# Kernel optimization log

Measured on AMD Instinct MI355X. Metric: run time of the kernel, lower is better.

Reference implementation:

```python
import jax, jax.numpy as jnp
import numpy as np

BANDWIDTH = 8.0

def setup_inputs() -> dict:
    key = jax.random.key(0)
    k1, k2 = jax.random.split(key)
    points = jax.random.normal(k1, (1, 8192, 32), dtype=jnp.float32)
    reference = jax.random.normal(k2, (1, 8192, 32), dtype=jnp.float32)
    return {"points": points, "reference": reference}

def reference(points, reference):
    # points: [B, N, D], reference: [B, M, D]
    # squared Euclidean distances via the expanded form to avoid the
    # O(B*N*M*D) difference tensor the original broadcasting would build
    x2 = jnp.sum(points * points, axis=-1)      # [B, N]
    y2 = jnp.sum(reference * reference, axis=-1)  # [B, M]
    xy = jnp.einsum('bnd,bmd->bnm', points, reference)  # [B, N, M]
    s_ij = x2[:, :, None] + y2[:, None, :] - 2.0 * xy   # [B, N, M]
    factor = jnp.float32(-1.0 / (2.0 * BANDWIDTH ** 2))
    k_ij = jnp.exp(s_ij * factor)               # [B, N, M] gaussian kernel
    nominator = jnp.einsum('bnm,bmd->bnd', k_ij, reference)
    denominator = jnp.sum(k_ij, axis=2, keepdims=True)  # [B, N, 1]
    return nominator / denominator
```

## Files before the change

kernel.cpp:

```cpp
#include <hip/hip_runtime.h>
#include <hip/hip_bf16.h>

#define D 32
#define FACTOR (-1.0f / 128.0f)
#define LOG2E  1.44269504088896340736f

typedef __attribute__((ext_vector_type(8)))  short bf16x8;
typedef __attribute__((ext_vector_type(16))) float f32x16;
typedef __attribute__((ext_vector_type(4)))  float f32x4;

#if __has_builtin(__builtin_amdgcn_exp2f)
#define EXP2(x) __builtin_amdgcn_exp2f(x)
#else
#define EXP2(x) exp2f(x)
#endif

__device__ __forceinline__ ushort bfr(float x) {
    __hip_bfloat16 h = __float2bfloat16(x);
    return *reinterpret_cast<ushort*>(&h);
}
__device__ __forceinline__ float bf2f(ushort u) {
    uint w = ((uint)u) << 16;
    return *reinterpret_cast<float*>(&w);
}
__device__ __forceinline__ uint pk2(float a, float b) {
    return (uint)bfr(a) | ((uint)bfr(b) << 16);
}

__global__ __launch_bounds__(256) void msk_prep(const float* __restrict__ X,
                                                const float* __restrict__ Y,
                                                ushort* __restrict__ Xb,
                                                ushort* __restrict__ Yb,
                                                ushort* __restrict__ yT,
                                                float* __restrict__ x2,
                                                float* __restrict__ y2,
                                                int N, int M) {
    const int t = blockIdx.x * 256 + threadIdx.x;
    const int i = t >> 2;
    const int c = t & 3;
    if (i >= N + M) return;
    const bool isX = (i < N);
    const int r = isX ? i : i - N;
    const float* src = (isX ? X : Y) + (size_t)r * D + c * 8;

    float4 va = *reinterpret_cast<const float4*>(src);
    float4 vb = *reinterpret_cast<const float4*>(src + 4);
    float f[8] = {va.x, va.y, va.z, va.w, vb.x, vb.y, vb.z, vb.w};

    ushort u[8];
    float s = 0.f;
#pragma unroll
    for (int k = 0; k < 8; ++k) {
        u[k] = bfr(f[k]);
        float g = bf2f(u[k]);
        s = fmaf(g, g, s);
    }
    s += __shfl_xor(s, 1);
    s += __shfl_xor(s, 2);

    uint w[4];
#pragma unroll
    for (int q = 0; q < 4; ++q) w[q] = (uint)u[2 * q] | ((uint)u[2 * q + 1] << 16);

    ushort* dstrow = (isX ? Xb : Yb) + (size_t)r * D + c * 8;
    *reinterpret_cast<uint4*>(dstrow) = *reinterpret_cast<const uint4*>(w);

    if (c == 0) (isX ? x2 : y2)[r] = s;

    if (!isX) {
#pragma unroll
        for (int k = 0; k < 8; ++k)
            yT[(size_t)(c * 8 + k) * M + r] = u[k];
    }
}

__global__ __launch_bounds__(256) void msk_main(const ushort* __restrict__ Xb,
                                                const ushort* __restrict__ Yb,
                                                const ushort* __restrict__ yT,
                                                const float* __restrict__ x2,
                                                const float* __restrict__ y2,
                                                float* __restrict__ pnom,
                                                float* __restrict__ pden,
                                                int N, int M, int chunk) {
    __shared__ uint4 lYb[2][64][4];
    __shared__ uint4 lYT[2][32][8];

    const int tid  = threadIdx.x;
    const int lane = tid & 63;
    const int wid  = tid >> 6;
    const int h    = lane >> 5;
    const int ln   = lane & 31;
    const int n0   = blockIdx.x * 128 + wid * 32;
    const int m0b  = blockIdx.y * chunk;
    const int ns   = chunk >> 6;

    const int rY = tid >> 2, cY = tid & 3;
    const int dT = tid >> 3, sT = tid & 7;

    const ushort* xrow = Xb + (size_t)(n0 + ln) * D + h * 8;
    const bf16x8 xf0 = *reinterpret_cast<const bf16x8*>(xrow);
    const bf16x8 xf1 = *reinterpret_cast<const bf16x8*>(xrow + 16);

    const float F2  = FACTOR * LOG2E;
    const float C2  = -2.0f * F2;
    const float xb2 = x2[n0 + ln] * F2;

    f32x16 nom = {};
    float den = 0.f;

    union Fu { uint u[4]; bf16x8 v; };

    uint4 ldYb, ldYT;
    auto issue_loads = [&](int step) {
        const int m = m0b + step * 64;
        ldYb = *(reinterpret_cast<const uint4*>(Yb + (size_t)(m + rY) * D) + cY);
        ldYT = *(reinterpret_cast<const uint4*>(yT + (size_t)dT * M + m) + sT);
    };
    auto stage = [&](int b) {
        lYb[b][rY][cY ^ (rY & 3)] = ldYb;
        lYT[b][dT][sT ^ (dT & 7)] = ldYT;
    };

    issue_loads(0);
    stage(0);
    if (ns > 1) issue_loads(1);

    for (int t = 0; t < ns; ++t) {
        __syncthreads();
        const int b  = t & 1;
        const int m0 = m0b + t * 64;

#pragma unroll
        for (int tA = 0; tA < 2; ++tA) {
            const int lr = tA * 32 + ln;
            const bf16x8 af0 = *reinterpret_cast<const bf16x8*>(
                &lYb[b][lr][(0 + h) ^ (ln & 3)]);
            const bf16x8 af1 = *reinterpret_cast<const bf16x8*>(
                &lYb[b][lr][(2 + h) ^ (ln & 3)]);

            f32x16 s = {};
            s = __builtin_amdgcn_mfma_f32_32x32x16_bf16(af0, xf0, s, 0, 0, 0);
            s = __builtin_amdgcn_mfma_f32_32x32x16_bf16(af1, xf1, s, 0, 0, 0);

            const int mt = m0 + tA * 32;
            uint pw[8];
#pragma unroll
            for (int r4 = 0; r4 < 4; ++r4) {
                f32x4 yv = *reinterpret_cast<const f32x4*>(y2 + mt + r4 * 8 + h * 4);
                float kq[4];
#pragma unroll
                for (int q = 0; q < 4; ++q)
                    kq[q] = EXP2(fmaf(s[r4 * 4 + q], C2, fmaf(yv[q], F2, xb2)));
                den += (kq[0] + kq[1]) + (kq[2] + kq[3]);
                pw[r4 * 2 + 0] = pk2(kq[0], kq[1]);
                pw[r4 * 2 + 1] = pk2(kq[2], kq[3]);
            }
            Fu pa0, pa1;
#pragma unroll
            for (int q = 0; q < 4; ++q) { pa0.u[q] = pw[q]; pa1.u[q] = pw[q + 4]; }

            const uint2* yr = reinterpret_cast<const uint2*>(&lYT[b][ln][0]);
            const int sw = ln & 7;
            Fu b0, b1;
            *reinterpret_cast<uint2*>(&b0.u[0]) = yr[((tA * 4 + 0) ^ sw) * 2 + h];
            *reinterpret_cast<uint2*>(&b0.u[2]) = yr[((tA * 4 + 1) ^ sw) * 2 + h];
            *reinterpret_cast<uint2*>(&b1.u[0]) = yr[((tA * 4 + 2) ^ sw) * 2 + h];
            *reinterpret_cast<uint2*>(&b1.u[2]) = yr[((tA * 4 + 3) ^ sw) * 2 + h];

            nom = __builtin_amdgcn_mfma_f32_32x32x16_bf16(pa0.v, b0.v, nom, 0, 0, 0);
            nom = __builtin_amdgcn_mfma_f32_32x32x16_bf16(pa1.v, b1.v, nom, 0, 0, 0);
        }

        if (t + 1 < ns) {
            stage((t + 1) & 1);
            if (t + 2 < ns) issue_loads(t + 2);
        }
    }

    den += __shfl_xor(den, 32);

    const size_t base = (size_t)blockIdx.y * N;
#pragma unroll
    for (int r = 0; r < 16; ++r) {
        const int row = (r & 3) + 8 * (r >> 2) + 4 * h;
        pnom[(base + n0 + row) * 32 + ln] = nom[r];
    }
    if (h == 0) pden[base + n0 + ln] = den;
}

__global__ __launch_bounds__(256) void msk_reduce(const float* __restrict__ pnom,
                                                  const float* __restrict__ pden,
                                                  float* __restrict__ out,
                                                  int N, int S) {
    const int t = blockIdx.x * blockDim.x + threadIdx.x;
    if (t >= N * 32) return;
    const int n = t >> 5;
    float nom = 0.f, den = 0.f;
    for (int s = 0; s < S; ++s) {
        nom += pnom[(size_t)s * N * 32 + t];
        den += pden[(size_t)s * N + n];
    }
    out[t] = nom / den;
}

extern "C" void kernel_launch(void* const* d_in, const int* in_sizes, int n_in,
                              void* d_out, int out_size, void* d_ws, size_t ws_size,
                              hipStream_t stream) {
    const float* X = (const float*)d_in[0];
    const float* Y = (const float*)d_in[1];
    float* out     = (float*)d_out;

    const int N = in_sizes[0] / D;
    const int M = in_sizes[1] / D;

    char* p = (char*)d_ws;
    ushort* Xb = (ushort*)p; p += (size_t)N * D * sizeof(ushort);
    ushort* Yb = (ushort*)p; p += (size_t)M * D * sizeof(ushort);
    ushort* yT = (ushort*)p; p += (size_t)M * D * sizeof(ushort);
    float*  x2 = (float*)p;  p += (size_t)N * sizeof(float);
    float*  y2 = (float*)p;  p += (size_t)M * sizeof(float);
    size_t used = (size_t)(p - (char*)d_ws);
    used = (used + 255) & ~(size_t)255;

    const size_t per_s = (size_t)N * 33 * sizeof(float);
    int S = 16;
    while (S > 1 && used + (size_t)S * per_s > ws_size) S >>= 1;
    const int chunk = M / S;

    float* pnom = (float*)((char*)d_ws + used);
    float* pden = pnom + (size_t)S * N * 32;

    msk_prep<<<dim3(((N + M) * 4 + 255) / 256), dim3(256), 0, stream>>>(
        X, Y, Xb, Yb, yT, x2, y2, N, M);

    msk_main<<<dim3(N / 128, S), dim3(256), 0, stream>>>(
        Xb, Yb, yT, x2, y2, pnom, pden, N, M, chunk);

    msk_reduce<<<dim3((N * 32 + 255) / 256), dim3(256), 0, stream>>>(
        pnom, pden, out, N, S);
}
```

Measured before the change: 91.41 us.

## Software-pipeline QK MFMA one tile ahead of exp and PV MFMA with setprio

Restructures the main loop so the distance GEMM for the next 64-row Y tile is issued right after the barrier, while the exp/pack and the numerator GEMM for the current tile run in between. Both 32-row subtiles are computed together, so their MFMAs are independent and interleaved. s_setprio raises wave priority around the MFMA bursts. The aim is to overlap matrix-core latency with the VALU exp work. The cost is higher register pressure from holding two extra accumulators (sA0/sA1).

```diff
diff --git a/kernel.cpp b/kernel.cpp
--- a/kernel.cpp
+++ b/kernel.cpp
@@ -107,7 +107,6 @@
 
     f32x16 nom = {};
     float den = 0.f;
-
     union Fu { uint u[4]; bf16x8 v; };
 
     uint4 ldYb, ldYT;
@@ -116,64 +115,88 @@
         ldYb = *(reinterpret_cast<const uint4*>(Yb + (size_t)(m + rY) * D) + cY);
         ldYT = *(reinterpret_cast<const uint4*>(yT + (size_t)dT * M + m) + sT);
     };
-    auto stage = [&](int b) {
-        lYb[b][rY][cY ^ (rY & 3)] = ldYb;
-        lYT[b][dT][sT ^ (dT & 7)] = ldYT;
+    auto stage = [&](int bb) {
+        lYb[bb][rY][cY ^ (rY & 3)] = ldYb;
+        lYT[bb][dT][sT ^ (dT & 7)] = ldYT;
+    };
+
+    f32x16 sA0, sA1;
+    auto gemm1 = [&](int bb) {
+        const bf16x8 a00 = *reinterpret_cast<const bf16x8*>(&lYb[bb][ln][(0 + h) ^ (ln & 3)]);
+        const bf16x8 a01 = *reinterpret_cast<const bf16x8*>(&lYb[bb][ln][(2 + h) ^ (ln & 3)]);
+        const bf16x8 a10 = *reinterpret_cast<const bf16x8*>(&lYb[bb][32 + ln][(0 + h) ^ (ln & 3)]);
+        const bf16x8 a11 = *reinterpret_cast<const bf16x8*>(&lYb[bb][32 + ln][(2 + h) ^ (ln & 3)]);
+        const f32x16 z = {};
+        __builtin_amdgcn_s_setprio(1);
+        sA0 = __builtin_amdgcn_mfma_f32_32x32x16_bf16(a00, xf0, z, 0, 0, 0);
+        sA1 = __builtin_amdgcn_mfma_f32_32x32x16_bf16(a10, xf0, z, 0, 0, 0);
+        sA0 = __builtin_amdgcn_mfma_f32_32x32x16_bf16(a01, xf1, sA0, 0, 0, 0);
+        sA1 = __builtin_amdgcn_mfma_f32_32x32x16_bf16(a11, xf1, sA1, 0, 0, 0);
+        __builtin_amdgcn_s_setprio(0);
+    };
+
+    auto expack = [&](const f32x16& s, int mt, uint* pw) {
+#pragma unroll
+        for (int r4 = 0; r4 < 4; ++r4) {
+            f32x4 yv = *reinterpret_cast<const f32x4*>(y2 + mt + r4 * 8 + h * 4);
+            float kq[4];
+#pragma unroll
+            for (int q = 0; q < 4; ++q)
+                kq[q] = EXP2(fmaf(s[r4 * 4 + q], C2, fmaf(yv[q], F2, xb2)));
+            den += (kq[0] + kq[1]) + (kq[2] + kq[3]);
+            pw[r4 * 2 + 0] = pk2(kq[0], kq[1]);
+            pw[r4 * 2 + 1] = pk2(kq[2], kq[3]);
+        }
     };
 
     issue_loads(0);
     stage(0);
     if (ns > 1) issue_loads(1);
+    __syncthreads();
+    gemm1(0);
 
     for (int t = 0; t < ns; ++t) {
-        __syncthreads();
         const int b  = t & 1;
         const int m0 = m0b + t * 64;
-
-#pragma unroll
-        for (int tA = 0; tA < 2; ++tA) {
-            const int lr = tA * 32 + ln;
-            const bf16x8 af0 = *reinterpret_cast<const bf16x8*>(
-                &lYb[b][lr][(0 + h) ^ (ln & 3)]);
-            const bf16x8 af1 = *reinterpret_cast<const bf16x8*>(
-                &lYb[b][lr][(2 + h) ^ (ln & 3)]);
-
-            f32x16 s = {};
-            s = __builtin_amdgcn_mfma_f32_32x32x16_bf16(af0, xf0, s, 0, 0, 0);
-            s = __builtin_amdgcn_mfma_f32_32x32x16_bf16(af1, xf1, s, 0, 0, 0);
-
-            const int mt = m0 + tA * 32;
-            uint pw[8];
-#pragma unroll
-            for (int r4 = 0; r4 < 4; ++r4) {
-                f32x4 yv = *reinterpret_cast<const f32x4*>(y2 + mt + r4 * 8 + h * 4);
-                float kq[4];
-#pragma unroll
-                for (int q = 0; q < 4; ++q)
-                    kq[q] = EXP2(fmaf(s[r4 * 4 + q], C2, fmaf(yv[q], F2, xb2)));
-                den += (kq[0] + kq[1]) + (kq[2] + kq[3]);
-                pw[r4 * 2 + 0] = pk2(kq[0], kq[1]);
-                pw[r4 * 2 + 1] = pk2(kq[2], kq[3]);
-            }
-            Fu pa0, pa1;
-#pragma unroll
-            for (int q = 0; q < 4; ++q) { pa0.u[q] = pw[q]; pa1.u[q] = pw[q + 4]; }
-
-            const uint2* yr = reinterpret_cast<const uint2*>(&lYT[b][ln][0]);
-            const int sw = ln & 7;
-            Fu b0, b1;
-            *reinterpret_cast<uint2*>(&b0.u[0]) = yr[((tA * 4 + 0) ^ sw) * 2 + h];
-            *reinterpret_cast<uint2*>(&b0.u[2]) = yr[((tA * 4 + 1) ^ sw) * 2 + h];
-            *reinterpret_cast<uint2*>(&b1.u[0]) = yr[((tA * 4 + 2) ^ sw) * 2 + h];
-            *reinterpret_cast<uint2*>(&b1.u[2]) = yr[((tA * 4 + 3) ^ sw) * 2 + h];
-
-            nom = __builtin_amdgcn_mfma_f32_32x32x16_bf16(pa0.v, b0.v, nom, 0, 0, 0);
-            nom = __builtin_amdgcn_mfma_f32_32x32x16_bf16(pa1.v, b1.v, nom, 0, 0, 0);
-        }
 
         if (t + 1 < ns) {
             stage((t + 1) & 1);
             if (t + 2 < ns) issue_loads(t + 2);
+        }
+
+        uint pw0[8], pw1[8];
+        expack(sA0, m0, pw0);
+        expack(sA1, m0 + 32, pw1);
+
+        Fu p00, p01, p10, p11;
+#pragma unroll
+        for (int q = 0; q < 4; ++q) {
+            p00.u[q] = pw0[q]; p01.u[q] = pw0[q + 4];
+            p10.u[q] = pw1[q]; p11.u[q] = pw1[q + 4];
+        }
+
+        const uint2* yr = reinterpret_cast<const uint2*>(&lYT[b][ln][0]);
+        const int sw = ln & 7;
+        Fu b00, b01, b10, b11;
+        *reinterpret_cast<uint2*>(&b00.u[0]) = yr[(0 ^ sw) * 2 + h];
+        *reinterpret_cast<uint2*>(&b00.u[2]) = yr[(1 ^ sw) * 2 + h];
+        *reinterpret_cast<uint2*>(&b01.u[0]) = yr[(2 ^ sw) * 2 + h];
+        *reinterpret_cast<uint2*>(&b01.u[2]) = yr[(3 ^ sw) * 2 + h];
+        *reinterpret_cast<uint2*>(&b10.u[0]) = yr[(4 ^ sw) * 2 + h];
+        *reinterpret_cast<uint2*>(&b10.u[2]) = yr[(5 ^ sw) * 2 + h];
+        *reinterpret_cast<uint2*>(&b11.u[0]) = yr[(6 ^ sw) * 2 + h];
+        *reinterpret_cast<uint2*>(&b11.u[2]) = yr[(7 ^ sw) * 2 + h];
+
+        __builtin_amdgcn_s_setprio(1);
+        nom = __builtin_amdgcn_mfma_f32_32x32x16_bf16(p00.v, b00.v, nom, 0, 0, 0);
+        nom = __builtin_amdgcn_mfma_f32_32x32x16_bf16(p01.v, b01.v, nom, 0, 0, 0);
+        nom = __builtin_amdgcn_mfma_f32_32x32x16_bf16(p10.v, b10.v, nom, 0, 0, 0);
+        nom = __builtin_amdgcn_mfma_f32_32x32x16_bf16(p11.v, b11.v, nom, 0, 0, 0);
+        __builtin_amdgcn_s_setprio(0);
+
+        if (t + 1 < ns) {
+            __syncthreads();
+            gemm1((t + 1) & 1);
         }
     }
 
```

Result: slower. 93.87 us (+2.7%).

## Drop cancelling x2 term, prescale y2, and double the per-step M tile

Applied to the files above, without the earlier changes.

Removes the per-row ||x||^2 term from the exponent, since it scales numerator and denominator by the same factor and cancels in the final ratio. The prep kernel now stores y2 already multiplied by the exp2 scale, saving one FMA per kernel element. The main loop processes 128 reference points per step instead of 64, with one barrier per step and staging of the next buffer placed before compute. Denominator accumulation is split into two partial sums. In exchange, LDS use doubles and the exponent values are no longer shifted by -x2, which slightly changes bf16 rounding and the range of the exp results.

```diff
diff --git a/kernel.cpp b/kernel.cpp
--- a/kernel.cpp
+++ b/kernel.cpp
@@ -32,8 +32,7 @@
                                                 ushort* __restrict__ Xb,
                                                 ushort* __restrict__ Yb,
                                                 ushort* __restrict__ yT,
-                                                float* __restrict__ x2,
-                                                float* __restrict__ y2,
+                                                float* __restrict__ y2s,
                                                 int N, int M) {
     const int t = blockIdx.x * 256 + threadIdx.x;
     const int i = t >> 2;
@@ -65,9 +64,8 @@
     ushort* dstrow = (isX ? Xb : Yb) + (size_t)r * D + c * 8;
     *reinterpret_cast<uint4*>(dstrow) = *reinterpret_cast<const uint4*>(w);
 
-    if (c == 0) (isX ? x2 : y2)[r] = s;
-
     if (!isX) {
+        if (c == 0) y2s[r] = s * (FACTOR * LOG2E);
 #pragma unroll
         for (int k = 0; k < 8; ++k)
             yT[(size_t)(c * 8 + k) * M + r] = u[k];
@@ -77,13 +75,12 @@
 __global__ __launch_bounds__(256) void msk_main(const ushort* __restrict__ Xb,
                                                 const ushort* __restrict__ Yb,
                                                 const ushort* __restrict__ yT,
-                                                const float* __restrict__ x2,
-                                                const float* __restrict__ y2,
+                                                const float* __restrict__ y2s,
                                                 float* __restrict__ pnom,
                                                 float* __restrict__ pden,
                                                 int N, int M, int chunk) {
-    __shared__ uint4 lYb[2][64][4];
-    __shared__ uint4 lYT[2][32][8];
+    __shared__ uint4 lYb[2][128][4];
+    __shared__ uint4 lYT[2][32][16];
 
     const int tid  = threadIdx.x;
     const int lane = tid & 63;
@@ -92,7 +89,7 @@
     const int ln   = lane & 31;
     const int n0   = blockIdx.x * 128 + wid * 32;
     const int m0b  = blockIdx.y * chunk;
-    const int ns   = chunk >> 6;
+    const int ns   = chunk >> 7;
 
     const int rY = tid >> 2, cY = tid & 3;
     const int dT = tid >> 3, sT = tid & 7;
@@ -101,66 +98,72 @@
     const bf16x8 xf0 = *reinterpret_cast<const bf16x8*>(xrow);
     const bf16x8 xf1 = *reinterpret_cast<const bf16x8*>(xrow + 16);
 
-    const float F2  = FACTOR * LOG2E;
-    const float C2  = -2.0f * F2;
-    const float xb2 = x2[n0 + ln] * F2;
+    const float C2 = -2.0f * (FACTOR * LOG2E);
 
     f32x16 nom = {};
-    float den = 0.f;
-
+    float den0 = 0.f, den1 = 0.f;
     union Fu { uint u[4]; bf16x8 v; };
 
-    uint4 ldYb, ldYT;
+    uint4 ldY0, ldY1, ldT0, ldT1;
     auto issue_loads = [&](int step) {
-        const int m = m0b + step * 64;
-        ldYb = *(reinterpret_cast<const uint4*>(Yb + (size_t)(m + rY) * D) + cY);
-        ldYT = *(reinterpret_cast<const uint4*>(yT + (size_t)dT * M + m) + sT);
+        const int m = m0b + step * 128;
+        ldY0 = (reinterpret_cast<const uint4*>(Yb + (size_t)(m + rY) * D))[cY];
+        ldY1 = (reinterpret_cast<const uint4*>(Yb + (size_t)(m + rY + 64) * D))[cY];
+        const uint4* tp = reinterpret_cast<const uint4*>(yT + (size_t)dT * M + m);
+        ldT0 = tp[sT];
+        ldT1 = tp[sT + 8];
     };
-    auto stage = [&](int b) {
-        lYb[b][rY][cY ^ (rY & 3)] = ldYb;
-        lYT[b][dT][sT ^ (dT & 7)] = ldYT;
+    auto stage = [&](int bb) {
+        lYb[bb][rY][cY ^ (rY & 3)]       = ldY0;
+        lYb[bb][rY + 64][cY ^ (rY & 3)]  = ldY1;
+        lYT[bb][dT][sT ^ (dT & 7)]       = ldT0;
+        lYT[bb][dT][(sT + 8) ^ (dT & 7)] = ldT1;
     };
 
     issue_loads(0);
     stage(0);
     if (ns > 1) issue_loads(1);
+    __syncthreads();
 
     for (int t = 0; t < ns; ++t) {
-        __syncthreads();
         const int b  = t & 1;
-        const int m0 = m0b + t * 64;
-
-#pragma unroll
-        for (int tA = 0; tA < 2; ++tA) {
+        const int m0 = m0b + t * 128;
+
+        if (t + 1 < ns) {
+            stage((t + 1) & 1);
+            if (t + 2 < ns) issue_loads(t + 2);
+        }
+
+        const int sw = ln & 7;
+        const uint2* yr = reinterpret_cast<const uint2*>(&lYT[b][ln][0]);
+
+#pragma unroll
+        for (int tA = 0; tA < 4; ++tA) {
             const int lr = tA * 32 + ln;
-            const bf16x8 af0 = *reinterpret_cast<const bf16x8*>(
-                &lYb[b][lr][(0 + h) ^ (ln & 3)]);
-            const bf16x8 af1 = *reinterpret_cast<const bf16x8*>(
-                &lYb[b][lr][(2 + h) ^ (ln & 3)]);
+            const bf16x8 af0 = *reinterpret_cast<const bf16x8*>(&lYb[b][lr][(0 + h) ^ (ln & 3)]);
+            const bf16x8 af1 = *reinterpret_cast<const bf16x8*>(&lYb[b][lr][(2 + h) ^ (ln & 3)]);
 
             f32x16 s = {};
             s = __builtin_amdgcn_mfma_f32_32x32x16_bf16(af0, xf0, s, 0, 0, 0);
             s = __builtin_amdgcn_mfma_f32_32x32x16_bf16(af1, xf1, s, 0, 0, 0);
 
             const int mt = m0 + tA * 32;
-            uint pw[8];
+            Fu pa0, pa1;
 #pragma unroll
             for (int r4 = 0; r4 < 4; ++r4) {
-                f32x4 yv = *reinterpret_cast<const f32x4*>(y2 + mt + r4 * 8 + h * 4);
+                f32x4 yv = *reinterpret_cast<const f32x4*>(y2s + mt + r4 * 8 + h * 4);
                 float kq[4];
 #pragma unroll
                 for (int q = 0; q < 4; ++q)
-                    kq[q] = EXP2(fmaf(s[r4 * 4 + q], C2, fmaf(yv[q], F2, xb2)));
-                den += (kq[0] + kq[1]) + (kq[2] + kq[3]);
-                pw[r4 * 2 + 0] = pk2(kq[0], kq[1]);
-                pw[r4 * 2 + 1] = pk2(kq[2], kq[3]);
+                    kq[q] = EXP2(fmaf(s[r4 * 4 + q], C2, yv[q]));
+                den0 += kq[0] + kq[1];
+                den1 += kq[2] + kq[3];
+                uint w0 = pk2(kq[0], kq[1]);
+                uint w1 = pk2(kq[2], kq[3]);
+                if (r4 < 2) { pa0.u[r4 * 2] = w0; pa0.u[r4 * 2 + 1] = w1; }
+                else        { pa1.u[(r4 - 2) * 2] = w0; pa1.u[(r4 - 2) * 2 + 1] = w1; }
             }
-            Fu pa0, pa1;
-#pragma unroll
-            for (int q = 0; q < 4; ++q) { pa0.u[q] = pw[q]; pa1.u[q] = pw[q + 4]; }
-
-            const uint2* yr = reinterpret_cast<const uint2*>(&lYT[b][ln][0]);
-            const int sw = ln & 7;
+
             Fu b0, b1;
             *reinterpret_cast<uint2*>(&b0.u[0]) = yr[((tA * 4 + 0) ^ sw) * 2 + h];
             *reinterpret_cast<uint2*>(&b0.u[2]) = yr[((tA * 4 + 1) ^ sw) * 2 + h];
@@ -171,12 +174,10 @@
             nom = __builtin_amdgcn_mfma_f32_32x32x16_bf16(pa1.v, b1.v, nom, 0, 0, 0);
         }
 
-        if (t + 1 < ns) {
-            stage((t + 1) & 1);
-            if (t + 2 < ns) issue_loads(t + 2);
-        }
-    }
-
+        __syncthreads();
+    }
+
+    float den = den0 + den1;
     den += __shfl_xor(den, 32);
 
     const size_t base = (size_t)blockIdx.y * N;
@@ -214,11 +215,10 @@
     const int M = in_sizes[1] / D;
 
     char* p = (char*)d_ws;
-    ushort* Xb = (ushort*)p; p += (size_t)N * D * sizeof(ushort);
-    ushort* Yb = (ushort*)p; p += (size_t)M * D * sizeof(ushort);
-    ushort* yT = (ushort*)p; p += (size_t)M * D * sizeof(ushort);
-    float*  x2 = (float*)p;  p += (size_t)N * sizeof(float);
-    float*  y2 = (float*)p;  p += (size_t)M * sizeof(float);
+    ushort* Xb  = (ushort*)p; p += (size_t)N * D * sizeof(ushort);
+    ushort* Yb  = (ushort*)p; p += (size_t)M * D * sizeof(ushort);
+    ushort* yT  = (ushort*)p; p += (size_t)M * D * sizeof(ushort);
+    float*  y2s = (float*)p;  p += (size_t)M * sizeof(float);
     size_t used = (size_t)(p - (char*)d_ws);
     used = (used + 255) & ~(size_t)255;
 
@@ -231,10 +231,10 @@
     float* pden = pnom + (size_t)S * N * 32;
 
     msk_prep<<<dim3(((N + M) * 4 + 255) / 256), dim3(256), 0, stream>>>(
-        X, Y, Xb, Yb, yT, x2, y2, N, M);
+        X, Y, Xb, Yb, yT, y2s, N, M);
 
     msk_main<<<dim3(N / 128, S), dim3(256), 0, stream>>>(
-        Xb, Yb, yT, x2, y2, pnom, pden, N, M, chunk);
+        Xb, Yb, yT, y2s, pnom, pden, N, M, chunk);
 
     msk_reduce<<<dim3((N * 32 + 255) / 256), dim3(256), 0, stream>>>(
         pnom, pden, out, N, S);
```

Measured after the change: 95.52 us. +4.5%, slower.
